# Kernel tuning notes

Measured on AMD Instinct MI355X. Metric: run time of the kernel, lower is better.

Reference implementation:

```python
import jax, jax.numpy as jnp
import numpy as np

N = 20000
E = 640000
D = 128
NORM_FACTOR = 100.0
LN_EPS = 1e-5


def _layer_norm(x, g, b):
    mu = jnp.mean(x, axis=-1, keepdims=True)
    var = jnp.var(x, axis=-1, keepdims=True)
    return (x - mu) * jax.lax.rsqrt(var + LN_EPS) * g + b


def setup_inputs() -> dict:
    key = jax.random.key(0)
    ks = jax.random.split(key, 16)

    def lin(k, fan_in, shape):
        bound = 1.0 / np.sqrt(fan_in)
        return jax.random.uniform(k, shape, jnp.float32, -bound, bound)

    h = jax.random.normal(ks[0], (N, D), jnp.float32)
    distances = jax.random.uniform(ks[1], (E, 1), jnp.float32)
    edges = jax.random.randint(ks[2], (2, E), 0, N, jnp.int64)
    node_mask = jnp.ones((N, 1), jnp.float32)
    edge_mask = jnp.ones((E, 1), jnp.float32)

    return {
        "h": h, "distances": distances, "node_mask": node_mask, "edge_mask": edge_mask,
        # linear: in->out
        "lin_w": lin(ks[3], D, (D, D)), "lin_b": lin(ks[4], D, (D,)),
        # att_mlp: (2D+1)->2D -> 2D->D -> D->1
        "att_w1": lin(ks[5], 2 * D + 1, (2 * D, 2 * D + 1)), "att_b1": lin(ks[5], 2 * D + 1, (2 * D,)),
        "att_w2": lin(ks[6], 2 * D, (D, 2 * D)), "att_b2": lin(ks[6], 2 * D, (D,)),
        "att_w3": lin(ks[7], D, (1, D)), "att_b3": lin(ks[7], D, (1,)),
        # node_mlp: D->D, LN, SiLU, D->D
        "nm_w1": lin(ks[8], D, (D, D)), "nm_b1": lin(ks[8], D, (D,)),
        "nm_ln_g": jnp.ones((D,), jnp.float32), "nm_ln_b": jnp.zeros((D,), jnp.float32),
        "nm_w2": lin(ks[9], D, (D, D)), "nm_b2": lin(ks[9], D, (D,)),
        # final LayerNorm
        "ln_g": jnp.ones((D,), jnp.float32), "ln_b": jnp.zeros((D,), jnp.float32),
        "edges": edges,
    }


def reference(h, distances, node_mask, edge_mask,
              lin_w, lin_b, att_w1, att_b1, att_w2, att_b2, att_w3, att_b3,
              nm_w1, nm_b1, nm_ln_g, nm_ln_b, nm_w2, nm_b2, ln_g, ln_b, edges):
    x = h @ lin_w.T + lin_b                                  # [N, D]
    row, col = edges[0], edges[1]
    x_row = x[row]                                           # [E, D]
    x_col = x[col]                                           # [E, D]

    # DenseAtt
    d = distances * edge_mask
    x_cat = jnp.concatenate([x_row, x_col, d], axis=1)       # [E, 2D+1]
    a = jax.nn.silu(x_cat @ att_w1.T + att_b1)
    a = jax.nn.silu(a @ att_w2.T + att_b2)
    att = jax.nn.sigmoid(a @ att_w3.T + att_b3) * edge_mask  # [E, 1]

    agg = x_col * att                                        # [E, D]
    out = jax.ops.segment_sum(agg, row, num_segments=N) / NORM_FACTOR

    # node_mlp + residual
    o = out @ nm_w1.T + nm_b1
    o = jax.nn.silu(_layer_norm(o, nm_ln_g, nm_ln_b))
    o = o @ nm_w2.T + nm_b2
    hh = o + x

    hh = _layer_norm(hh, ln_g, ln_b)
    hh = jax.nn.silu(hh)                                     # act = SiLU
    return hh
```

## Files before the change

kernel.cpp:

```cpp
#include <hip/hip_runtime.h>
#include <hip/hip_bf16.h>

#define N_NODES 20000
#define E_EDGES 640000
#define DIM 128
#define CAP 96
#define EPB 64
#define NPB 8
#define XST 264

typedef __attribute__((ext_vector_type(8))) short bf16x8;
typedef __attribute__((ext_vector_type(4))) float f32x4;

#define LOG2E 1.44269504f
__device__ __forceinline__ float fsilu(float x) {
    return x * __builtin_amdgcn_rcpf(1.f + __builtin_amdgcn_exp2f(-LOG2E * x));
}
__device__ __forceinline__ float fsig(float x) {
    return __builtin_amdgcn_rcpf(1.f + __builtin_amdgcn_exp2f(-LOG2E * x));
}

__device__ __forceinline__ unsigned short f2bf(float x) {
    union { float f; unsigned u; } v; v.f = x;
    unsigned r = (v.u + 0x7fffu + ((v.u >> 16) & 1u)) >> 16;
    return (unsigned short)r;
}
__device__ __forceinline__ float bf2f(unsigned short s) {
    union { unsigned u; float f; } v; v.u = ((unsigned)s) << 16;
    return v.f;
}
__device__ __forceinline__ unsigned pack_bf16(float lo, float hi) {
    union { float f; unsigned u; } a, b; a.f = lo; b.f = hi;
    unsigned ul = a.u + 0x8000u, uh = b.u + 0x8000u;
    return __builtin_amdgcn_perm(uh, ul, 0x07060302u);
}

#define PRE_PREP_BLOCKS 64
#define PRE_LIN_BLOCKS  625
#define PRE_ADJ_BLOCKS  2500
__global__ __launch_bounds__(256) void pre_kernel(
    const float* __restrict__ w1, const float* __restrict__ w2,
    unsigned short* __restrict__ w1b, float* __restrict__ w1p,
    unsigned short* __restrict__ w2b,
    const float* __restrict__ h, const float* __restrict__ lw,
    const float* __restrict__ lb, float* __restrict__ x,
    unsigned short* __restrict__ xb,
    const int* __restrict__ edges,
    const float* __restrict__ dist, const float* __restrict__ emask,
    int* __restrict__ cnt,
    int* __restrict__ adjc, float2* __restrict__ dm, int E) {
    __shared__ float hs[32][128];
    int b = blockIdx.x;
    int t = threadIdx.x;

    if (b < PRE_PREP_BLOCKS) {
        int i = b * 256 + t;
        const int stride = PRE_PREP_BLOCKS * 256;
        for (int idx = i; idx < 256 * 256; idx += stride) {
            int o = idx >> 8, k = idx & 255;
            w1b[idx] = f2bf(w1[o * 257 + k]);
        }
        for (int idx = i; idx < 128 * 256; idx += stride) {
            int n2 = idx >> 8, p = idx & 255;
            int bb = p & ~31, off = p & 31;
            int ksrc = bb + (off >> 1) + ((off & 1) << 4);
            w2b[idx] = f2bf(w2[n2 * 256 + ksrc]);
        }
        for (int idx = i; idx < 256; idx += stride) {
            int bb = idx & ~31, off = idx & 31;
            int ksrc = bb + (off >> 1) + ((off & 1) << 4);
            w1p[idx] = w1[ksrc * 257 + 256];
        }
    } else if (b < PRE_PREP_BLOCKS + PRE_LIN_BLOCKS) {
        int nb = b - PRE_PREP_BLOCKS;
        int n0 = nb * 32;
        int ch = t & 127, g = t >> 7;
#pragma unroll
        for (int j = 0; j < 16; ++j) hs[g * 16 + j][ch] = h[(size_t)(n0 + g * 16 + j) * DIM + ch];
        __syncthreads();
        float acc[16];
#pragma unroll
        for (int j = 0; j < 16; ++j) acc[j] = 0.f;
        for (int kc = 0; kc < 128; kc += 4) {
            float4 wv = *(const float4*)&lw[(size_t)ch * DIM + kc];
#pragma unroll
            for (int j = 0; j < 16; ++j)
                acc[j] += wv.x * hs[g * 16 + j][kc] + wv.y * hs[g * 16 + j][kc + 1]
                        + wv.z * hs[g * 16 + j][kc + 2] + wv.w * hs[g * 16 + j][kc + 3];
        }
        float bias = lb[ch];
#pragma unroll
        for (int j = 0; j < 16; ++j) {
            float v = acc[j] + bias;
            int n = n0 + g * 16 + j;
            x[(size_t)n * DIM + ch] = v;
            xb[(size_t)n * DIM + ch] = f2bf(v);
        }
    } else {
        int e = (b - PRE_PREP_BLOCKS - PRE_LIN_BLOCKS) * 256 + t;
        if (e < E) {
            int r = edges[e];
            int col = edges[E + e];
            int slot = atomicAdd(&cnt[r], 1);
            if (slot < CAP) {
                adjc[(size_t)r * CAP + slot] = col;
                float em = emask[e];
                float2 de; de.x = dist[e] * em; de.y = em;
                dm[(size_t)r * CAP + slot] = de;
            }
        }
    }
}

#define PRC_NPB 16
__global__ __launch_bounds__(256) void prc_kernel(
    const unsigned short* __restrict__ xb,
    const unsigned short* __restrict__ w1b,
    const float* __restrict__ b1,
    float* __restrict__ prf, unsigned short* __restrict__ pcb) {
    int n0 = blockIdx.x * PRC_NPB;
    int w = threadIdx.x >> 6, lane = threadIdx.x & 63;
    int lrow = lane & 15, quad = lane >> 4;

    bf16x8 a[4];
#pragma unroll
    for (int kk = 0; kk < 4; ++kk)
        a[kk] = *(const bf16x8*)&xb[(size_t)(n0 + lrow) * DIM + kk * 32 + quad * 8];

    f32x4 z = {0.f, 0.f, 0.f, 0.f};
#pragma unroll
    for (int i = 0; i < 8; ++i) {
        int gt = w * 8 + i;
        int half = gt >> 4;
        int obase = (gt & 15) * 16;
        f32x4 acc = z;
#pragma unroll
        for (int kk = 0; kk < 4; ++kk) {
            bf16x8 bfrag = *(const bf16x8*)&w1b[(size_t)(obase + lrow) * 256 + half * 128 + kk * 32 + quad * 8];
            acc = __builtin_amdgcn_mfma_f32_16x16x32_bf16(a[kk], bfrag, acc, 0, 0, 0);
        }
        int o = obase + lrow;
        if (half == 0) {
            float bias = b1[o];
#pragma unroll
            for (int r = 0; r < 4; ++r)
                prf[(size_t)(n0 + quad * 4 + r) * 256 + o] = acc[r] + bias;
        } else {
#pragma unroll
            for (int r = 0; r < 4; ++r)
                pcb[(size_t)(n0 + quad * 4 + r) * 256 + o] = f2bf(acc[r]);
        }
    }
}

__global__ __launch_bounds__(512, 4) void edge_kernel(
    const float* __restrict__ prf, const unsigned short* __restrict__ pcb,
    const float2* __restrict__ dm, const int* __restrict__ adjc,
    const int* __restrict__ cnt,
    const float* __restrict__ w1p,
    const unsigned short* __restrict__ w2b, const float* __restrict__ b2,
    const float* __restrict__ w3, const float* __restrict__ b3v,
    float* __restrict__ attA) {
    __shared__ unsigned short buf[EPB * XST];
    __shared__ float part[8][EPB];
    __shared__ float w1ps[256];
    __shared__ unsigned short list[NPB * CAP];
    __shared__ int offs[NPB + 1];
    __shared__ int cnts[NPB];
    __shared__ int cidx_s[EPB], jj_s[EPB];
    __shared__ float dv_s[EPB], em_s[EPB];

    int tid = threadIdx.x;
    int n0 = blockIdx.x * NPB;

    if (tid < NPB) { int c = cnt[n0 + tid]; cnts[tid] = c > CAP ? CAP : c; }
    if (tid >= 256 && tid < 512) w1ps[tid - 256] = w1p[tid - 256];
    __syncthreads();
    if (tid == 0) {
        int s = 0;
#pragma unroll
        for (int j = 0; j < NPB; ++j) { offs[j] = s; s += cnts[j]; }
        offs[NPB] = s;
    }
    __syncthreads();
    {
        int jg = tid >> 5, l = tid & 31;
        if (jg < NPB) {
            int c = cnts[jg], o = offs[jg];
            for (int i = l; i < c; i += 32) list[o + i] = (unsigned short)((jg << 8) | i);
        }
    }
    int count = offs[NPB];
    int ntiles = (count + EPB - 1) / EPB;
    __syncthreads();

    int wave = tid >> 6, lane = tid & 63;
    int lrow = lane & 15, quad = lane >> 4;
    int n2 = wave * 16 + lrow;
    float bias2 = b2[n2];
    float w3v = w3[n2];
    float b3s = b3v[0];

    f32x4 zz = {0.f, 0.f, 0.f, 0.f};

    for (int t = 0; t < ntiles; ++t) {
        if (tid < EPB) {
            int s = t * EPB + tid;
            if (s < count) {
                int ji = list[s];
                int j = ji >> 8, i = ji & 255;
                size_t ai = (size_t)(n0 + j) * CAP + i;
                float2 de = dm[ai];
                jj_s[tid] = j; cidx_s[tid] = adjc[ai];
                dv_s[tid] = de.x; em_s[tid] = de.y;
            } else {
                jj_s[tid] = 0; cidx_s[tid] = 0;
                dv_s[tid] = 0.f; em_s[tid] = 0.f;
            }
        }
        __syncthreads();

        {
            int ge = tid >> 3, cb = tid & 7;
            const unsigned short* pcp = pcb + (size_t)cidx_s[ge] * 256 + cb * 32;
            const float* prow = prf + (size_t)(n0 + jj_s[ge]) * 256 + cb * 32;
            float d = dv_s[ge];
            unsigned* wrow = (unsigned*)&buf[ge * XST + cb * 32];
            const float* wp = &w1ps[cb * 32];

            float pa[8], pb[8];
            *(float4*)&pa[0] = *(const float4*)&prow[0];
            *(float4*)&pa[4] = *(const float4*)&prow[4];
            *(float4*)&pb[0] = *(const float4*)&prow[16];
            *(float4*)&pb[4] = *(const float4*)&prow[20];
            bf16x8 qA = *(const bf16x8*)&pcp[0];
            bf16x8 qB = *(const bf16x8*)&pcp[16];
#pragma unroll
            for (int l = 0; l < 8; ++l) {
                float s0 = pa[l] + bf2f((unsigned short)qA[l]) + d * wp[2 * l];
                float s1 = pb[l] + bf2f((unsigned short)qB[l]) + d * wp[2 * l + 1];
                wrow[l] = pack_bf16(fsilu(s0), fsilu(s1));
            }
            *(float4*)&pa[0] = *(const float4*)&prow[8];
            *(float4*)&pa[4] = *(const float4*)&prow[12];
            *(float4*)&pb[0] = *(const float4*)&prow[24];
            *(float4*)&pb[4] = *(const float4*)&prow[28];
            qA = *(const bf16x8*)&pcp[8];
            qB = *(const bf16x8*)&pcp[24];
#pragma unroll
            for (int l = 0; l < 8; ++l) {
                float s0 = pa[l] + bf2f((unsigned short)qA[l]) + d * wp[16 + 2 * l];
                float s1 = pb[l] + bf2f((unsigned short)qB[l]) + d * wp[16 + 2 * l + 1];
                wrow[8 + l] = pack_bf16(fsilu(s0), fsilu(s1));
            }
        }
        __syncthreads();

        f32x4 acc2[4];
#pragma unroll
        for (int mt = 0; mt < 4; ++mt) acc2[mt] = zz;

        for (int kk = 0; kk < 8; ++kk) {
            int ka = kk * 32 + quad * 8;
            bf16x8 bfrag = *(const bf16x8*)&w2b[(size_t)n2 * 256 + ka];
#pragma unroll
            for (int mt = 0; mt < 4; ++mt) {
                bf16x8 a = *(bf16x8*)&buf[(mt * 16 + lrow) * XST + ka];
                acc2[mt] = __builtin_amdgcn_mfma_f32_16x16x32_bf16(a, bfrag, acc2[mt], 0, 0, 0);
            }
        }

        float s[4][4];
#pragma unroll
        for (int mt = 0; mt < 4; ++mt)
#pragma unroll
            for (int r = 0; r < 4; ++r)
                s[mt][r] = fsilu(acc2[mt][r] + bias2) * w3v;
#pragma unroll
        for (int off = 1; off < 16; off <<= 1) {
#pragma unroll
            for (int mt = 0; mt < 4; ++mt)
#pragma unroll
                for (int r = 0; r < 4; ++r)
                    s[mt][r] += __shfl_xor(s[mt][r], off);
        }
        if (lrow == 0) {
#pragma unroll
            for (int mt = 0; mt < 4; ++mt)
#pragma unroll
                for (int r = 0; r < 4; ++r)
                    part[wave][mt * 16 + quad * 4 + r] = s[mt][r];
        }
        __syncthreads();

        if (tid < EPB) {
            int sidx = t * EPB + tid;
            if (sidx < count) {
                float ssum = b3s;
#pragma unroll
                for (int w = 0; w < 8; ++w) ssum += part[w][tid];
                int ji = list[sidx];
                int j = ji >> 8, i = ji & 255;
                attA[(size_t)(n0 + j) * CAP + i] = fsig(ssum) * em_s[tid];
            }
        }
    }
}

__global__ __launch_bounds__(256) void node_kernel(
    const float* __restrict__ attA, const int* __restrict__ adjc, const int* __restrict__ cnt,
    const unsigned short* __restrict__ xb,
    const float* __restrict__ x,
    const float* __restrict__ w1, const float* __restrict__ bb1,
    const float* __restrict__ lng, const float* __restrict__ lnb,
    const float* __restrict__ w2, const float* __restrict__ bb2,
    const float* __restrict__ gF, const float* __restrict__ bF,
    float* __restrict__ out, int E) {
    __shared__ float atts[NPB][CAP];
    __shared__ int   cols[NPB][CAP];
    __shared__ float outv[NPB][128];
    __shared__ float bufs[NPB][128];
    __shared__ float mu_s[NPB], rs_s[NPB];
    __shared__ int cnts[NPB];

    int t = threadIdx.x;
    int n0 = blockIdx.x * NPB;

    if (t < NPB) { int c = cnt[n0 + t]; cnts[t] = c > CAP ? CAP : c; }
    __syncthreads();

    {
        int jg = t >> 5, l = t & 31;
        int c = cnts[jg];
        const int* al = adjc + (size_t)(n0 + jg) * CAP;
        const float* av = attA + (size_t)(n0 + jg) * CAP;
        for (int i = l; i < c; i += 32) {
            atts[jg][i] = av[i];
            cols[jg][i] = al[i];
        }
    }
    __syncthreads();

    int w = t >> 6, lane = t & 63;
#pragma unroll
    for (int jj = 0; jj < 2; ++jj) {
        int j = w * 2 + jj;
        int c = cnts[j];
        float lo0 = 0.f, hi0 = 0.f, lo1 = 0.f, hi1 = 0.f;
        float lo2 = 0.f, hi2 = 0.f, lo3 = 0.f, hi3 = 0.f;
        int i = 0;
        for (; i + 3 < c; i += 4) {
            unsigned u0 = *(const unsigned*)&xb[(size_t)cols[j][i]     * DIM + lane * 2];
            unsigned u1 = *(const unsigned*)&xb[(size_t)cols[j][i + 1] * DIM + lane * 2];
            unsigned u2 = *(const unsigned*)&xb[(size_t)cols[j][i + 2] * DIM + lane * 2];
            unsigned u3 = *(const unsigned*)&xb[(size_t)cols[j][i + 3] * DIM + lane * 2];
            float w0 = atts[j][i], w1v = atts[j][i + 1], w2v = atts[j][i + 2], w3v = atts[j][i + 3];
            lo0 += w0 * bf2f((unsigned short)(u0 & 0xffff)); hi0 += w0 * bf2f((unsigned short)(u0 >> 16));
            lo1 += w1v * bf2f((unsigned short)(u1 & 0xffff)); hi1 += w1v * bf2f((unsigned short)(u1 >> 16));
            lo2 += w2v * bf2f((unsigned short)(u2 & 0xffff)); hi2 += w2v * bf2f((unsigned short)(u2 >> 16));
            lo3 += w3v * bf2f((unsigned short)(u3 & 0xffff)); hi3 += w3v * bf2f((unsigned short)(u3 >> 16));
        }
        for (; i < c; ++i) {
            unsigned u0 = *(const unsigned*)&xb[(size_t)cols[j][i] * DIM + lane * 2];
            float w0 = atts[j][i];
            lo0 += w0 * bf2f((unsigned short)(u0 & 0xffff));
            hi0 += w0 * bf2f((unsigned short)(u0 >> 16));
        }
        outv[j][lane * 2]     = ((lo0 + lo1) + (lo2 + lo3)) * 0.01f;
        outv[j][lane * 2 + 1] = ((hi0 + hi1) + (hi2 + hi3)) * 0.01f;
    }
    __syncthreads();

    int h = t >> 7, ch = t & 127;
    float xres[4];
#pragma unroll
    for (int jj = 0; jj < 4; ++jj)
        xres[jj] = x[(size_t)(n0 + h * 4 + jj) * DIM + ch];

    float a1[4] = {0, 0, 0, 0};
    for (int kc = 0; kc < 128; kc += 4) {
        float4 wv = *(const float4*)&w1[(size_t)ch * DIM + kc];
#pragma unroll
        for (int jj = 0; jj < 4; ++jj) {
            int j = h * 4 + jj;
            a1[jj] += wv.x * outv[j][kc] + wv.y * outv[j][kc + 1] + wv.z * outv[j][kc + 2] + wv.w * outv[j][kc + 3];
        }
    }
    float bias1 = bb1[ch];
#pragma unroll
    for (int jj = 0; jj < 4; ++jj) bufs[h * 4 + jj][ch] = a1[jj] + bias1;
    __syncthreads();

    {
        int j = t >> 5, l = t & 31;
        float s = 0.f, qq = 0.f;
#pragma unroll
        for (int i = 0; i < 4; ++i) { float v = bufs[j][l + 32 * i]; s += v; qq += v * v; }
#pragma unroll
        for (int off = 16; off; off >>= 1) { s += __shfl_xor(s, off); qq += __shfl_xor(qq, off); }
        if (l == 0) {
            float mu = s * (1.f / 128.f);
            float var = qq * (1.f / 128.f) - mu * mu;
            mu_s[j] = mu; rs_s[j] = __builtin_amdgcn_rsqf(var + 1e-5f);
        }
    }
    __syncthreads();

    float g = lng[ch], bb = lnb[ch];
    float h2[4];
#pragma unroll
    for (int jj = 0; jj < 4; ++jj) {
        int j = h * 4 + jj;
        h2[jj] = fsilu((bufs[j][ch] - mu_s[j]) * rs_s[j] * g + bb);
    }
    __syncthreads();
#pragma unroll
    for (int jj = 0; jj < 4; ++jj) bufs[h * 4 + jj][ch] = h2[jj];
    __syncthreads();

    float a3[4] = {0, 0, 0, 0};
    for (int kc = 0; kc < 128; kc += 4) {
        float4 wv = *(const float4*)&w2[(size_t)ch * DIM + kc];
#pragma unroll
        for (int jj = 0; jj < 4; ++jj) {
            int j = h * 4 + jj;
            a3[jj] += wv.x * bufs[j][kc] + wv.y * bufs[j][kc + 1] + wv.z * bufs[j][kc + 2] + wv.w * bufs[j][kc + 3];
        }
    }
    float bias2 = bb2[ch];
    float hh[4];
#pragma unroll
    for (int jj = 0; jj < 4; ++jj) hh[jj] = a3[jj] + bias2 + xres[jj];
    __syncthreads();
#pragma unroll
    for (int jj = 0; jj < 4; ++jj) bufs[h * 4 + jj][ch] = hh[jj];
    __syncthreads();

    {
        int j = t >> 5, l = t & 31;
        float s = 0.f, qq = 0.f;
#pragma unroll
        for (int i = 0; i < 4; ++i) { float v = bufs[j][l + 32 * i]; s += v; qq += v * v; }
#pragma unroll
        for (int off = 16; off; off >>= 1) { s += __shfl_xor(s, off); qq += __shfl_xor(qq, off); }
        if (l == 0) {
            float mu = s * (1.f / 128.f);
            float var = qq * (1.f / 128.f) - mu * mu;
            mu_s[j] = mu; rs_s[j] = __builtin_amdgcn_rsqf(var + 1e-5f);
        }
    }
    __syncthreads();

    float gf = gF[ch], bf = bF[ch];
#pragma unroll
    for (int jj = 0; jj < 4; ++jj) {
        int j = h * 4 + jj;
        float y = (hh[jj] - mu_s[j]) * rs_s[j] * gf + bf;
        out[(size_t)(n0 + j) * DIM + ch] = fsilu(y);
    }
}

extern "C" void kernel_launch(void* const* d_in, const int* in_sizes, int n_in,
                              void* d_out, int out_size, void* d_ws, size_t ws_size,
                              hipStream_t stream) {
    const float* h         = (const float*)d_in[0];
    const float* distances = (const float*)d_in[1];
    const float* edge_mask = (const float*)d_in[3];
    const float* lin_w     = (const float*)d_in[4];
    const float* lin_b     = (const float*)d_in[5];
    const float* att_w1    = (const float*)d_in[6];
    const float* att_b1    = (const float*)d_in[7];
    const float* att_w2    = (const float*)d_in[8];
    const float* att_b2    = (const float*)d_in[9];
    const float* att_w3    = (const float*)d_in[10];
    const float* att_b3    = (const float*)d_in[11];
    const float* nm_w1     = (const float*)d_in[12];
    const float* nm_b1     = (const float*)d_in[13];
    const float* nm_ln_g   = (const float*)d_in[14];
    const float* nm_ln_b   = (const float*)d_in[15];
    const float* nm_w2     = (const float*)d_in[16];
    const float* nm_b2     = (const float*)d_in[17];
    const float* ln_g      = (const float*)d_in[18];
    const float* ln_b      = (const float*)d_in[19];
    const int*   edges     = (const int*)d_in[20];
    float* out = (float*)d_out;

    const int N = N_NODES, E = E_EDGES;

    char* ws = (char*)d_ws;
    float* x            = (float*)ws;            ws += (size_t)N * DIM * 4;
    unsigned short* xb  = (unsigned short*)ws;   ws += (size_t)N * DIM * 2;
    int* cnt            = (int*)ws;              ws += (size_t)N * 4;
    int* adjc           = (int*)ws;              ws += (size_t)N * CAP * 4;
    float2* dm          = (float2*)ws;           ws += (size_t)N * CAP * 8;
    float* attA         = (float*)ws;            ws += (size_t)N * CAP * 4;
    unsigned short* w1b = (unsigned short*)ws;   ws += 256 * 256 * 2;
    float* w1p          = (float*)ws;            ws += 256 * 4;
    unsigned short* w2b = (unsigned short*)ws;   ws += 128 * 256 * 2;
    float* prf          = (float*)ws;            ws += (size_t)N * 256 * 4;
    unsigned short* pcb = (unsigned short*)ws;   ws += (size_t)N * 256 * 2;

    hipMemsetAsync(cnt, 0, (size_t)N * 4, stream);

    pre_kernel<<<PRE_PREP_BLOCKS + PRE_LIN_BLOCKS + PRE_ADJ_BLOCKS, 256, 0, stream>>>(
        att_w1, att_w2, w1b, w1p, w2b,
        h, lin_w, lin_b, x, xb,
        edges, distances, edge_mask, cnt, adjc, dm, E);
    prc_kernel<<<N / PRC_NPB, 256, 0, stream>>>(xb, w1b, att_b1, prf, pcb);
    edge_kernel<<<N / NPB, 512, 0, stream>>>(prf, pcb, dm, adjc, cnt,
                                             w1p, w2b, att_b2,
                                             att_w3, att_b3, attA);
    node_kernel<<<N / NPB, 256, 0, stream>>>(attA, adjc, cnt, xb, x,
                                             nm_w1, nm_b1, nm_ln_g, nm_ln_b,
                                             nm_w2, nm_b2, ln_g, ln_b, out, E);
}
```

Measured before the change: 478.9 us.

## Flatten edges via global prefix scan so edge kernel processes fixed 64-edge tiles

Replaces per-node-group edge blocks, which loop over a variable number of partial tiles, with a global exclusive scan of degrees and a flattened CSR-ordered edge array. Each edge_kernel block then handles exactly 64 contiguous edges with no tile loop or partial-tile waste. The flat-array build is fused into the same launch as the prc GEMM. This adds a single-block scan kernel and an extra 16-byte-per-edge flat buffer write and read in exchange for full MFMA tiles and better load balance.

After: 461.4 us. 3.7% less time.

```diff
diff --git a/kernel.cpp b/kernel.cpp
--- a/kernel.cpp
+++ b/kernel.cpp
@@ -45,10 +45,8 @@
     const float* __restrict__ h, const float* __restrict__ lw,
     const float* __restrict__ lb, float* __restrict__ x,
     unsigned short* __restrict__ xb,
-    const int* __restrict__ edges,
-    const float* __restrict__ dist, const float* __restrict__ emask,
-    int* __restrict__ cnt,
-    int* __restrict__ adjc, float2* __restrict__ dm, int E) {
+    const int* __restrict__ edges, int* __restrict__ cnt,
+    int2* __restrict__ adj2, int E) {
     __shared__ float hs[32][128];
     int b = blockIdx.x;
     int t = threadIdx.x;
@@ -102,213 +100,230 @@
             int r = edges[e];
             int col = edges[E + e];
             int slot = atomicAdd(&cnt[r], 1);
-            if (slot < CAP) {
-                adjc[(size_t)r * CAP + slot] = col;
-                float em = emask[e];
-                float2 de; de.x = dist[e] * em; de.y = em;
-                dm[(size_t)r * CAP + slot] = de;
-            }
-        }
-    }
-}
-
-#define PRC_NPB 16
-__global__ __launch_bounds__(256) void prc_kernel(
+            if (slot < CAP) { int2 v; v.x = e; v.y = col; adj2[(size_t)r * CAP + slot] = v; }
+        }
+    }
+}
+
+__global__ __launch_bounds__(1024) void scan_kernel(const int* __restrict__ cnt,
+                                                    int* __restrict__ off) {
+    __shared__ int part[1024];
+    int t = threadIdx.x;
+    int base = t * 20;
+    int loc[20];
+    int s = 0;
+#pragma unroll
+    for (int i = 0; i < 20; ++i) {
+        int idx = base + i;
+        int v = 0;
+        if (idx < N_NODES) { v = cnt[idx]; v = v > CAP ? CAP : v; }
+        loc[i] = s; s += v;
+    }
+    part[t] = s;
+    __syncthreads();
+    int run = s;
+    for (int d = 1; d < 1024; d <<= 1) {
+        int v = (t >= d) ? part[t - d] : 0;
+        __syncthreads();
+        part[t] += v;
+        __syncthreads();
+    }
+    int ex = part[t] - run;
+#pragma unroll
+    for (int i = 0; i < 20; ++i) {
+        int idx = base + i;
+        if (idx < N_NODES) off[idx] = ex + loc[i];
+    }
+    if (t == 1023) off[N_NODES] = part[1023];
+}
+
+#define MID_PRC_BLOCKS 1250
+#define MID_FLAT_BLOCKS 2500
+__global__ __launch_bounds__(256) void mid_kernel(
     const unsigned short* __restrict__ xb,
     const unsigned short* __restrict__ w1b,
     const float* __restrict__ b1,
-    float* __restrict__ prf, unsigned short* __restrict__ pcb) {
-    int n0 = blockIdx.x * PRC_NPB;
-    int w = threadIdx.x >> 6, lane = threadIdx.x & 63;
-    int lrow = lane & 15, quad = lane >> 4;
-
-    bf16x8 a[4];
-#pragma unroll
-    for (int kk = 0; kk < 4; ++kk)
-        a[kk] = *(const bf16x8*)&xb[(size_t)(n0 + lrow) * DIM + kk * 32 + quad * 8];
-
-    f32x4 z = {0.f, 0.f, 0.f, 0.f};
-#pragma unroll
-    for (int i = 0; i < 8; ++i) {
-        int gt = w * 8 + i;
-        int half = gt >> 4;
-        int obase = (gt & 15) * 16;
-        f32x4 acc = z;
-#pragma unroll
-        for (int kk = 0; kk < 4; ++kk) {
-            bf16x8 bfrag = *(const bf16x8*)&w1b[(size_t)(obase + lrow) * 256 + half * 128 + kk * 32 + quad * 8];
-            acc = __builtin_amdgcn_mfma_f32_16x16x32_bf16(a[kk], bfrag, acc, 0, 0, 0);
-        }
-        int o = obase + lrow;
-        if (half == 0) {
-            float bias = b1[o];
-#pragma unroll
-            for (int r = 0; r < 4; ++r)
-                prf[(size_t)(n0 + quad * 4 + r) * 256 + o] = acc[r] + bias;
-        } else {
-#pragma unroll
-            for (int r = 0; r < 4; ++r)
-                pcb[(size_t)(n0 + quad * 4 + r) * 256 + o] = f2bf(acc[r]);
+    float* __restrict__ prf, unsigned short* __restrict__ pcb,
+    const int2* __restrict__ adj2, const int* __restrict__ cnt,
+    const int* __restrict__ off,
+    const float* __restrict__ dist, const float* __restrict__ emask,
+    int4* __restrict__ flat) {
+    int b = blockIdx.x;
+    if (b < MID_PRC_BLOCKS) {
+        int n0 = b * 16;
+        int w = threadIdx.x >> 6, lane = threadIdx.x & 63;
+        int lrow = lane & 15, quad = lane >> 4;
+
+        bf16x8 a[4];
+#pragma unroll
+        for (int kk = 0; kk < 4; ++kk)
+            a[kk] = *(const bf16x8*)&xb[(size_t)(n0 + lrow) * DIM + kk * 32 + quad * 8];
+
+        f32x4 z = {0.f, 0.f, 0.f, 0.f};
+#pragma unroll
+        for (int i = 0; i < 8; ++i) {
+            int gt = w * 8 + i;
+            int half = gt >> 4;
+            int obase = (gt & 15) * 16;
+            f32x4 acc = z;
+#pragma unroll
+            for (int kk = 0; kk < 4; ++kk) {
+                bf16x8 bfrag = *(const bf16x8*)&w1b[(size_t)(obase + lrow) * 256 + half * 128 + kk * 32 + quad * 8];
+                acc = __builtin_amdgcn_mfma_f32_16x16x32_bf16(a[kk], bfrag, acc, 0, 0, 0);
+            }
+            int o = obase + lrow;
+            if (half == 0) {
+                float bias = b1[o];
+#pragma unroll
+                for (int r = 0; r < 4; ++r)
+                    prf[(size_t)(n0 + quad * 4 + r) * 256 + o] = acc[r] + bias;
+            } else {
+#pragma unroll
+                for (int r = 0; r < 4; ++r)
+                    pcb[(size_t)(n0 + quad * 4 + r) * 256 + o] = f2bf(acc[r]);
+            }
+        }
+    } else {
+        int fb = b - MID_PRC_BLOCKS;
+        int n0 = fb * NPB;
+        int jg = threadIdx.x >> 5, l = threadIdx.x & 31;
+        int n = n0 + jg;
+        int c = cnt[n]; c = c > CAP ? CAP : c;
+        int o = off[n];
+        const int2* al = adj2 + (size_t)n * CAP;
+        for (int i = l; i < c; i += 32) {
+            int2 v = al[i];
+            float em = emask[v.x];
+            float dv = dist[v.x] * em;
+            int4 wv;
+            union { float f; int i; } u1, u2; u1.f = dv; u2.f = em;
+            wv.x = n; wv.y = v.y; wv.z = u1.i; wv.w = u2.i;
+            flat[o + i] = wv;
         }
     }
 }
 
 __global__ __launch_bounds__(512, 4) void edge_kernel(
     const float* __restrict__ prf, const unsigned short* __restrict__ pcb,
-    const float2* __restrict__ dm, const int* __restrict__ adjc,
-    const int* __restrict__ cnt,
+    const int4* __restrict__ flat, const int* __restrict__ off,
     const float* __restrict__ w1p,
     const unsigned short* __restrict__ w2b, const float* __restrict__ b2,
     const float* __restrict__ w3, const float* __restrict__ b3v,
-    float* __restrict__ attA) {
+    float* __restrict__ attv) {
     __shared__ unsigned short buf[EPB * XST];
     __shared__ float part[8][EPB];
     __shared__ float w1ps[256];
-    __shared__ unsigned short list[NPB * CAP];
-    __shared__ int offs[NPB + 1];
-    __shared__ int cnts[NPB];
-    __shared__ int cidx_s[EPB], jj_s[EPB];
-    __shared__ float dv_s[EPB], em_s[EPB];
+    __shared__ float dvals[EPB], emv[EPB];
+    __shared__ int ridx[EPB], cidx[EPB];
 
     int tid = threadIdx.x;
-    int n0 = blockIdx.x * NPB;
-
-    if (tid < NPB) { int c = cnt[n0 + tid]; cnts[tid] = c > CAP ? CAP : c; }
-    if (tid >= 256 && tid < 512) w1ps[tid - 256] = w1p[tid - 256];
-    __syncthreads();
-    if (tid == 0) {
-        int s = 0;
-#pragma unroll
-        for (int j = 0; j < NPB; ++j) { offs[j] = s; s += cnts[j]; }
-        offs[NPB] = s;
-    }
-    __syncthreads();
-    {
-        int jg = tid >> 5, l = tid & 31;
-        if (jg < NPB) {
-            int c = cnts[jg], o = offs[jg];
-            for (int i = l; i < c; i += 32) list[o + i] = (unsigned short)((jg << 8) | i);
-        }
-    }
-    int count = offs[NPB];
-    int ntiles = (count + EPB - 1) / EPB;
-    __syncthreads();
+    int eb = blockIdx.x * EPB;
+
+    if (tid < EPB) {
+        int count = off[N_NODES];
+        int idx = eb + tid;
+        int4 v;
+        if (idx < count) v = flat[idx];
+        else { v.x = 0; v.y = 0; v.z = 0; v.w = 0; }
+        ridx[tid] = v.x; cidx[tid] = v.y;
+        union { int i; float f; } a, bu; a.i = v.z; bu.i = v.w;
+        dvals[tid] = a.f; emv[tid] = bu.f;
+    }
+    if (tid >= 64 && tid < 320) w1ps[tid - 64] = w1p[tid - 64];
 
     int wave = tid >> 6, lane = tid & 63;
     int lrow = lane & 15, quad = lane >> 4;
     int n2 = wave * 16 + lrow;
     float bias2 = b2[n2];
     float w3v = w3[n2];
-    float b3s = b3v[0];
+
+    __syncthreads();
+
+    {
+        int ge = tid >> 3, cb = tid & 7;
+        const float* prow = prf + (size_t)ridx[ge] * 256 + cb * 32;
+        const unsigned short* pcp = pcb + (size_t)cidx[ge] * 256 + cb * 32;
+        float d = dvals[ge];
+        unsigned* wrow = (unsigned*)&buf[ge * XST + cb * 32];
+        const float* wp = &w1ps[cb * 32];
+
+        float pa[8], pb[8];
+        *(float4*)&pa[0] = *(const float4*)&prow[0];
+        *(float4*)&pa[4] = *(const float4*)&prow[4];
+        *(float4*)&pb[0] = *(const float4*)&prow[16];
+        *(float4*)&pb[4] = *(const float4*)&prow[20];
+        bf16x8 qA = *(const bf16x8*)&pcp[0];
+        bf16x8 qB = *(const bf16x8*)&pcp[16];
+#pragma unroll
+        for (int l = 0; l < 8; ++l) {
+            float s0 = pa[l] + bf2f((unsigned short)qA[l]) + d * wp[2 * l];
+            float s1 = pb[l] + bf2f((unsigned short)qB[l]) + d * wp[2 * l + 1];
+            wrow[l] = pack_bf16(fsilu(s0), fsilu(s1));
+        }
+        *(float4*)&pa[0] = *(const float4*)&prow[8];
+        *(float4*)&pa[4] = *(const float4*)&prow[12];
+        *(float4*)&pb[0] = *(const float4*)&prow[24];
+        *(float4*)&pb[4] = *(const float4*)&prow[28];
+        qA = *(const bf16x8*)&pcp[8];
+        qB = *(const bf16x8*)&pcp[24];
+#pragma unroll
+        for (int l = 0; l < 8; ++l) {
+            float s0 = pa[l] + bf2f((unsigned short)qA[l]) + d * wp[16 + 2 * l];
+            float s1 = pb[l] + bf2f((unsigned short)qB[l]) + d * wp[16 + 2 * l + 1];
+            wrow[8 + l] = pack_bf16(fsilu(s0), fsilu(s1));
+        }
+    }
+    __syncthreads();
 
     f32x4 zz = {0.f, 0.f, 0.f, 0.f};
-
-    for (int t = 0; t < ntiles; ++t) {
-        if (tid < EPB) {
-            int s = t * EPB + tid;
-            if (s < count) {
-                int ji = list[s];
-                int j = ji >> 8, i = ji & 255;
-                size_t ai = (size_t)(n0 + j) * CAP + i;
-                float2 de = dm[ai];
-                jj_s[tid] = j; cidx_s[tid] = adjc[ai];
-                dv_s[tid] = de.x; em_s[tid] = de.y;
-            } else {
-                jj_s[tid] = 0; cidx_s[tid] = 0;
-                dv_s[tid] = 0.f; em_s[tid] = 0.f;
-            }
-        }
-        __syncthreads();
-
-        {
-            int ge = tid >> 3, cb = tid & 7;
-            const unsigned short* pcp = pcb + (size_t)cidx_s[ge] * 256 + cb * 32;
-            const float* prow = prf + (size_t)(n0 + jj_s[ge]) * 256 + cb * 32;
-            float d = dv_s[ge];
-            unsigned* wrow = (unsigned*)&buf[ge * XST + cb * 32];
-            const float* wp = &w1ps[cb * 32];
-
-            float pa[8], pb[8];
-            *(float4*)&pa[0] = *(const float4*)&prow[0];
-            *(float4*)&pa[4] = *(const float4*)&prow[4];
-            *(float4*)&pb[0] = *(const float4*)&prow[16];
-            *(float4*)&pb[4] = *(const float4*)&prow[20];
-            bf16x8 qA = *(const bf16x8*)&pcp[0];
-            bf16x8 qB = *(const bf16x8*)&pcp[16];
-#pragma unroll
-            for (int l = 0; l < 8; ++l) {
-                float s0 = pa[l] + bf2f((unsigned short)qA[l]) + d * wp[2 * l];
-                float s1 = pb[l] + bf2f((unsigned short)qB[l]) + d * wp[2 * l + 1];
-                wrow[l] = pack_bf16(fsilu(s0), fsilu(s1));
-            }
-            *(float4*)&pa[0] = *(const float4*)&prow[8];
-            *(float4*)&pa[4] = *(const float4*)&prow[12];
-            *(float4*)&pb[0] = *(const float4*)&prow[24];
-            *(float4*)&pb[4] = *(const float4*)&prow[28];
-            qA = *(const bf16x8*)&pcp[8];
-            qB = *(const bf16x8*)&pcp[24];
-#pragma unroll
-            for (int l = 0; l < 8; ++l) {
-                float s0 = pa[l] + bf2f((unsigned short)qA[l]) + d * wp[16 + 2 * l];
-                float s1 = pb[l] + bf2f((unsigned short)qB[l]) + d * wp[16 + 2 * l + 1];
-                wrow[8 + l] = pack_bf16(fsilu(s0), fsilu(s1));
-            }
-        }
-        __syncthreads();
-
-        f32x4 acc2[4];
-#pragma unroll
-        for (int mt = 0; mt < 4; ++mt) acc2[mt] = zz;
-
-        for (int kk = 0; kk < 8; ++kk) {
-            int ka = kk * 32 + quad * 8;
-            bf16x8 bfrag = *(const bf16x8*)&w2b[(size_t)n2 * 256 + ka];
-#pragma unroll
-            for (int mt = 0; mt < 4; ++mt) {
-                bf16x8 a = *(bf16x8*)&buf[(mt * 16 + lrow) * XST + ka];
-                acc2[mt] = __builtin_amdgcn_mfma_f32_16x16x32_bf16(a, bfrag, acc2[mt], 0, 0, 0);
-            }
-        }
-
-        float s[4][4];
+    f32x4 acc2[4];
+#pragma unroll
+    for (int mt = 0; mt < 4; ++mt) acc2[mt] = zz;
+
+    for (int kk = 0; kk < 8; ++kk) {
+        int ka = kk * 32 + quad * 8;
+        bf16x8 bfrag = *(const bf16x8*)&w2b[(size_t)n2 * 256 + ka];
+#pragma unroll
+        for (int mt = 0; mt < 4; ++mt) {
+            bf16x8 a = *(bf16x8*)&buf[(mt * 16 + lrow) * XST + ka];
+            acc2[mt] = __builtin_amdgcn_mfma_f32_16x16x32_bf16(a, bfrag, acc2[mt], 0, 0, 0);
+        }
+    }
+
+    float s[4][4];
+#pragma unroll
+    for (int mt = 0; mt < 4; ++mt)
+#pragma unroll
+        for (int r = 0; r < 4; ++r)
+            s[mt][r] = fsilu(acc2[mt][r] + bias2) * w3v;
+#pragma unroll
+    for (int off2 = 1; off2 < 16; off2 <<= 1) {
 #pragma unroll
         for (int mt = 0; mt < 4; ++mt)
 #pragma unroll
             for (int r = 0; r < 4; ++r)
-                s[mt][r] = fsilu(acc2[mt][r] + bias2) * w3v;
-#pragma unroll
-        for (int off = 1; off < 16; off <<= 1) {
-#pragma unroll
-            for (int mt = 0; mt < 4; ++mt)
-#pragma unroll
-                for (int r = 0; r < 4; ++r)
-                    s[mt][r] += __shfl_xor(s[mt][r], off);
-        }
-        if (lrow == 0) {
-#pragma unroll
-            for (int mt = 0; mt < 4; ++mt)
-#pragma unroll
-                for (int r = 0; r < 4; ++r)
-                    part[wave][mt * 16 + quad * 4 + r] = s[mt][r];
-        }
-        __syncthreads();
-
-        if (tid < EPB) {
-            int sidx = t * EPB + tid;
-            if (sidx < count) {
-                float ssum = b3s;
-#pragma unroll
-                for (int w = 0; w < 8; ++w) ssum += part[w][tid];
-                int ji = list[sidx];
-                int j = ji >> 8, i = ji & 255;
-                attA[(size_t)(n0 + j) * CAP + i] = fsig(ssum) * em_s[tid];
-            }
-        }
+                s[mt][r] += __shfl_xor(s[mt][r], off2);
+    }
+    if (lrow == 0) {
+#pragma unroll
+        for (int mt = 0; mt < 4; ++mt)
+#pragma unroll
+            for (int r = 0; r < 4; ++r)
+                part[wave][mt * 16 + quad * 4 + r] = s[mt][r];
+    }
+    __syncthreads();
+
+    if (tid < EPB) {
+        float ssum = b3v[0];
+#pragma unroll
+        for (int w = 0; w < 8; ++w) ssum += part[w][tid];
+        attv[eb + tid] = fsig(ssum) * emv[tid];
     }
 }
 
 __global__ __launch_bounds__(256) void node_kernel(
-    const float* __restrict__ attA, const int* __restrict__ adjc, const int* __restrict__ cnt,
+    const float* __restrict__ attv, const int2* __restrict__ adj2,
+    const int* __restrict__ cnt, const int* __restrict__ off,
     const unsigned short* __restrict__ xb,
     const float* __restrict__ x,
     const float* __restrict__ w1, const float* __restrict__ bb1,
@@ -332,11 +347,11 @@
     {
         int jg = t >> 5, l = t & 31;
         int c = cnts[jg];
-        const int* al = adjc + (size_t)(n0 + jg) * CAP;
-        const float* av = attA + (size_t)(n0 + jg) * CAP;
+        const int2* al = adj2 + (size_t)(n0 + jg) * CAP;
+        const float* av = attv + off[n0 + jg];
         for (int i = l; i < c; i += 32) {
             atts[jg][i] = av[i];
-            cols[jg][i] = al[i];
+            cols[jg][i] = al[i].y;
         }
     }
     __syncthreads();
@@ -397,7 +412,7 @@
 #pragma unroll
         for (int i = 0; i < 4; ++i) { float v = bufs[j][l + 32 * i]; s += v; qq += v * v; }
 #pragma unroll
-        for (int off = 16; off; off >>= 1) { s += __shfl_xor(s, off); qq += __shfl_xor(qq, off); }
+        for (int off2 = 16; off2; off2 >>= 1) { s += __shfl_xor(s, off2); qq += __shfl_xor(qq, off2); }
         if (l == 0) {
             float mu = s * (1.f / 128.f);
             float var = qq * (1.f / 128.f) - mu * mu;
@@ -442,7 +457,7 @@
 #pragma unroll
         for (int i = 0; i < 4; ++i) { float v = bufs[j][l + 32 * i]; s += v; qq += v * v; }
 #pragma unroll
-        for (int off = 16; off; off >>= 1) { s += __shfl_xor(s, off); qq += __shfl_xor(qq, off); }
+        for (int off2 = 16; off2; off2 >>= 1) { s += __shfl_xor(s, off2); qq += __shfl_xor(qq, off2); }
         if (l == 0) {
             float mu = s * (1.f / 128.f);
             float var = qq * (1.f / 128.f) - mu * mu;
@@ -491,26 +506,29 @@
     float* x            = (float*)ws;            ws += (size_t)N * DIM * 4;
     unsigned short* xb  = (unsigned short*)ws;   ws += (size_t)N * DIM * 2;
     int* cnt            = (int*)ws;              ws += (size_t)N * 4;
-    int* adjc           = (int*)ws;              ws += (size_t)N * CAP * 4;
-    float2* dm          = (float2*)ws;           ws += (size_t)N * CAP * 8;
-    float* attA         = (float*)ws;            ws += (size_t)N * CAP * 4;
+    int* off            = (int*)ws;              ws += (size_t)(N + 4) * 4;
+    int2* adj2          = (int2*)ws;             ws += (size_t)N * CAP * 8;
+    float* attv         = (float*)ws;            ws += (size_t)E * 4;
     unsigned short* w1b = (unsigned short*)ws;   ws += 256 * 256 * 2;
     float* w1p          = (float*)ws;            ws += 256 * 4;
     unsigned short* w2b = (unsigned short*)ws;   ws += 128 * 256 * 2;
     float* prf          = (float*)ws;            ws += (size_t)N * 256 * 4;
     unsigned short* pcb = (unsigned short*)ws;   ws += (size_t)N * 256 * 2;
+    int4* flat          = (int4*)ws;             ws += (size_t)E * 16;
 
     hipMemsetAsync(cnt, 0, (size_t)N * 4, stream);
 
     pre_kernel<<<PRE_PREP_BLOCKS + PRE_LIN_BLOCKS + PRE_ADJ_BLOCKS, 256, 0, stream>>>(
         att_w1, att_w2, w1b, w1p, w2b,
         h, lin_w, lin_b, x, xb,
-        edges, distances, edge_mask, cnt, adjc, dm, E);
-    prc_kernel<<<N / PRC_NPB, 256, 0, stream>>>(xb, w1b, att_b1, prf, pcb);
-    edge_kernel<<<N / NPB, 512, 0, stream>>>(prf, pcb, dm, adjc, cnt,
+        edges, cnt, adj2, E);
+    scan_kernel<<<1, 1024, 0, stream>>>(cnt, off);
+    mid_kernel<<<MID_PRC_BLOCKS + MID_FLAT_BLOCKS, 256, 0, stream>>>(
+        xb, w1b, att_b1, prf, pcb, adj2, cnt, off, distances, edge_mask, flat);
+    edge_kernel<<<E / EPB, 512, 0, stream>>>(prf, pcb, flat, off,
                                              w1p, w2b, att_b2,
-                                             att_w3, att_b3, attA);
-    node_kernel<<<N / NPB, 256, 0, stream>>>(attA, adjc, cnt, xb, x,
+                                             att_w3, att_b3, attv);
+    node_kernel<<<N / NPB, 256, 0, stream>>>(attv, adj2, cnt, off, xb, x,
                                              nm_w1, nm_b1, nm_ln_g, nm_ln_b,
                                              nm_w2, nm_b2, ln_g, ln_b, out, E);
 }
```
